# Optimization experiments

Measured on AMD Instinct MI355X. Metric: run time of the kernel, lower is better.

## Reference

```python
import jax, jax.numpy as jnp
import numpy as np

B, S, D, H = 32, 1024, 192, 8
DH = D // H  # 24


def setup_inputs() -> dict:
    key = jax.random.key(0)
    ks = jax.random.split(key, 8)
    s_in = 1.0 / np.sqrt(D)
    return {
        "x": jax.random.normal(ks[0], (B, S, D), dtype=jnp.float32),
        "mask": jax.random.randint(ks[1], (B, S), 0, 2).astype(bool),
        "Wq": jax.random.normal(ks[2], (H, D, DH), dtype=jnp.float32) * s_in,
        "bq": jnp.zeros((H, DH), dtype=jnp.float32),
        "Wk": jax.random.normal(ks[3], (H, D, DH), dtype=jnp.float32) * s_in,
        "bk": jnp.zeros((H, DH), dtype=jnp.float32),
        "Wv": jax.random.normal(ks[4], (H, D, DH), dtype=jnp.float32) * s_in,
        "bv": jnp.zeros((H, DH), dtype=jnp.float32),
        "Wo": jax.random.normal(ks[5], (D, D), dtype=jnp.float32) * s_in,
        "bo": jnp.zeros((D,), dtype=jnp.float32),
    }


def reference(x, mask, Wq, bq, Wk, bk, Wv, bv, Wo, bo):
    # Batched per-head projections: [B,S,D] x [H,D,DH] -> [B,H,S,DH]
    q = jnp.einsum("bsd,hde->bhse", x, Wq) + bq[None, :, None, :]
    k = jnp.einsum("bsd,hde->bhse", x, Wk) + bk[None, :, None, :]
    v = jnp.einsum("bsd,hde->bhse", x, Wv) + bv[None, :, None, :]
    scale = 1.0 / np.sqrt(DH).astype(np.float32)
    scores = jnp.einsum("bhse,bhte->bhst", q, k) * scale  # [B,H,S,S]
    # mask [B,S] broadcast over heads and query positions (masked_fill with -1e9)
    scores = jnp.where(mask[:, None, None, :], scores, -1e9)
    weights = jax.nn.softmax(scores, axis=-1)
    out = jnp.einsum("bhst,bhte->bhse", weights, v)  # [B,H,S,DH]
    # concat heads along last dim -> [B,S,D]
    out = out.transpose(0, 2, 1, 3).reshape(B, S, D)
    return out @ Wo + bo
```

## Files before the change

### kernel.cpp

```cpp
#include <hip/hip_runtime.h>

typedef __attribute__((ext_vector_type(8))) short short8;
typedef __attribute__((ext_vector_type(4))) short short4v;
typedef __attribute__((ext_vector_type(4))) float f32x4;
typedef __attribute__((ext_vector_type(16))) float f32x16;
typedef __attribute__((ext_vector_type(2))) unsigned uint2v;
typedef __attribute__((ext_vector_type(4))) unsigned uint4v;

#define MFMA16(a,b,c) __builtin_amdgcn_mfma_f32_16x16x32_bf16((a),(b),(c),0,0,0)
#define MFMA32(a,b,c) __builtin_amdgcn_mfma_f32_32x32x16_bf16((a),(b),(c),0,0,0)

#define BB 32
#define SS 1024
#define DD 192
#define HH 8
#define DHP 32

#define SCALE_Q 0.294468266742895f

__device__ __forceinline__ short nb(float f) {
    __bf16 h = (__bf16)f;
    return __builtin_bit_cast(short, h);
}
__device__ __forceinline__ float bf2f(short s) {
    union { unsigned u; float f; } v; v.u = ((unsigned)(unsigned short)s) << 16;
    return v.f;
}
__device__ __forceinline__ unsigned pk2(float a, float b) {
    unsigned short lo = __builtin_bit_cast(unsigned short, (__bf16)a);
    unsigned short hi = __builtin_bit_cast(unsigned short, (__bf16)b);
    return (unsigned)lo | ((unsigned)hi << 16);
}

__global__ __launch_bounds__(256) void prep_kernel(
    const float* __restrict__ Wq, const float* __restrict__ Wk, const float* __restrict__ Wv,
    const float* __restrict__ Wo,
    short* __restrict__ WqF, short* __restrict__ WkF, short* __restrict__ WvF,
    short* __restrict__ WoFh, short* __restrict__ WoFl)
{
    int idx = blockIdx.x * 256 + threadIdx.x;
    const int NWX   = 3 * HH * DHP * DD;
    const int NWO   = DD * DD;
    if (idx < NWX) {
        int j = idx;
        int mat = j / (HH * DHP * DD);
        int jj  = j % (HH * DHP * DD);
        int h   = jj / (DHP * DD);
        int rem = jj % (DHP * DD);
        int e   = rem / DD;
        int d   = rem % DD;
        const float* W = (mat == 0) ? Wq : (mat == 1) ? Wk : Wv;
        short* WF      = (mat == 0) ? WqF : (mat == 1) ? WkF : WvF;
        float val = (e < 24) ? W[(h * DD + d) * 24 + e] : 0.f;
        int nt = e & 1, cc = e >> 1;
        int kk = d >> 5, g = (d >> 3) & 3, ee = d & 7;
        WF[(size_t)((((h*2+nt)*6 + kk)*64) + g*16 + cc)*8 + ee] = nb(val);
    } else if (idx < NWX + NWO) {
        int j = idx - NWX;
        int n = j / DD, k = j % DD;
        float f = Wo[k * DD + n];
        short hi = nb(f);
        int nn = n >> 4, cc = n & 15;
        int kk = k >> 5, g = (k >> 3) & 3, ee = k & 7;
        size_t addr = (size_t)(((nn*6 + kk)*64) + g*16 + cc)*8 + ee;
        WoFh[addr] = hi;
        WoFl[addr] = nb(f - bf2f(hi));
    }
}

__global__ __launch_bounds__(1024) void scan_kernel(
    const void* __restrict__ mask_raw,
    float* __restrict__ maskf, int* __restrict__ inv, int* __restrict__ cnt)
{
    int b = blockIdx.x, t = threadIdx.x;
    int lane = t & 63, wv = t >> 6;
    int idx = b * SS + t;

    const unsigned* mw = (const unsigned*)mask_raw;
    bool all01 = true, allf = true;
    #pragma unroll
    for (int i = 0; i < 16; i++) {
        unsigned w = mw[i];
        all01 = all01 && (w <= 1u);
        allf  = allf  && (w == 0u || w == 0x3F800000u);
    }
    bool m;
    if (all01)      m = (mw[idx] != 0u);
    else if (allf)  m = (((const float*)mask_raw)[idx] != 0.f);
    else            m = (((const unsigned char*)mask_raw)[idx] != 0);
    maskf[idx] = m ? 1.f : 0.f;

    unsigned long long bal = __ballot(m);
    int preU  = __popcll(bal & ((1ull << lane) - 1ull));
    int waveU = __popcll(bal);
    __shared__ int wsu[16];
    if (lane == 0) wsu[wv] = waveU;
    __syncthreads();
    int waveOffU = 0, totalU = 0;
    #pragma unroll
    for (int i = 0; i < 16; i++) {
        int v = wsu[i];
        if (i < wv) waveOffU += v;
        totalU += v;
    }
    int posU = waveOffU + preU;
    int posM = totalU + (wv * 64 - waveOffU) + (lane - preU);
    inv[idx] = m ? posU : posM;
    if (t == 0) cnt[b] = totalU;
}

__global__ __launch_bounds__(256) void proj_kernel(
    const float* __restrict__ x,
    const float* __restrict__ bq, const float* __restrict__ bk, const float* __restrict__ bv,
    const short* __restrict__ WqF, const short* __restrict__ WkF, const short* __restrict__ WvF,
    const float* __restrict__ maskf, const int* __restrict__ inv,
    short* __restrict__ Q, short* __restrict__ K, short* __restrict__ Vc)
{
    int tid = threadIdx.x;
    int lane = tid & 63, w = tid >> 6;
    int c = lane & 15, g = lane >> 4;
    int r0 = blockIdx.x * 64 + w * 16;
    int arow = r0 + c;
    int h0 = blockIdx.y * 2;

    int b_ = r0 >> 10;
    int s0 = (r0 & 1023) + g * 4;

    short8 a[6];
    #pragma unroll
    for (int kk = 0; kk < 6; kk++) {
        const float* px = x + (size_t)arow * DD + kk * 32 + g * 8;
        float4 f0 = *(const float4*)px;
        float4 f1 = *(const float4*)(px + 4);
        short8 t;
        t[0]=nb(f0.x); t[1]=nb(f0.y); t[2]=nb(f0.z); t[3]=nb(f0.w);
        t[4]=nb(f1.x); t[5]=nb(f1.y); t[6]=nb(f1.z); t[7]=nb(f1.w);
        a[kk] = t;
    }

    float mrow[4];
    int dst[4];
    #pragma unroll
    for (int r = 0; r < 4; r++) {
        mrow[r] = maskf[b_ * SS + s0 + r];
        dst[r]  = inv[b_ * SS + s0 + r];
    }

    #pragma unroll
    for (int hh = 0; hh < 2; hh++) {
        int h = h0 + hh;
        int bh = b_ * HH + h;
        #pragma unroll
        for (int mat = 0; mat < 3; mat++) {
            const short* WF   = (mat==0)?WqF:(mat==1)?WkF:WvF;
            const float* bias = (mat==0)?bq:(mat==1)?bk:bv;

            f32x4 acc0 = {0.f,0.f,0.f,0.f};
            f32x4 acc1 = {0.f,0.f,0.f,0.f};
            const short* Wp0 = WF + (size_t)((h*2+0)*6) * 512 + lane * 8;
            const short* Wp1 = WF + (size_t)((h*2+1)*6) * 512 + lane * 8;
            #pragma unroll
            for (int kk = 0; kk < 6; kk++) {
                short8 b0 = *(const short8*)(Wp0 + kk * 512);
                short8 b1 = *(const short8*)(Wp1 + kk * 512);
                acc0 = MFMA16(a[kk], b0, acc0);
                acc1 = MFMA16(a[kk], b1, acc1);
            }
            float bv0 = 0.f, bv1 = 0.f;
            if (2*c < 24) {
                float2 bb = *(const float2*)(bias + h * 24 + 2 * c);
                bv0 = bb.x; bv1 = bb.y;
            }

            if (mat == 0) {
                #pragma unroll
                for (int r = 0; r < 4; r++) {
                    float v0 = (acc0[r] + bv0) * SCALE_Q;
                    float v1 = (c == 15) ? 1.0f : (acc1[r] + bv1) * SCALE_Q;
                    *(unsigned*)(Q + ((size_t)bh * SS + s0 + r) * DHP + 2*c) = pk2(v0, v1);
                }
            } else if (mat == 1) {
                #pragma unroll
                for (int r = 0; r < 4; r++) {
                    float v0 = acc0[r] + bv0;
                    float v1 = (c == 15) ? ((mrow[r] != 0.f) ? 0.f : -1e30f)
                                         : (acc1[r] + bv1);
                    *(unsigned*)(K + ((size_t)bh * SS + dst[r]) * DHP + 2*c) = pk2(v0, v1);
                }
            } else {
                #pragma unroll
                for (int r = 0; r < 4; r++) {
                    float v0 = (c == 12) ? 1.0f : (acc0[r] + bv0);
                    float v1 = acc1[r] + bv1;
                    *(unsigned*)(Vc + ((size_t)bh * SS + dst[r]) * DHP + 2*c) = pk2(v0, v1);
                }
            }
        }
    }
}

__global__ __launch_bounds__(256) void vtrans_kernel(
    const short* __restrict__ Vc, short* __restrict__ Vt)
{
    __shared__ short tile[256][33];
    int bh = blockIdx.x, c4 = blockIdx.y;
    int t = threadIdx.x;
    const short* src = Vc + ((size_t)bh * SS + c4 * 256 + t) * DHP;
    short8 a0 = *(const short8*)(src);
    short8 a1 = *(const short8*)(src + 8);
    short8 a2 = *(const short8*)(src + 16);
    short8 a3 = *(const short8*)(src + 24);
    #pragma unroll
    for (int i = 0; i < 8; i++) {
        tile[t][i]      = a0[i];
        tile[t][8 + i]  = a1[i];
        tile[t][16 + i] = a2[i];
        tile[t][24 + i] = a3[i];
    }
    __syncthreads();
    int e = t & 31, jg = t >> 5;
    if (e < 25) {
        short* dstp = Vt + ((size_t)bh * DHP + e) * SS + c4 * 256 + jg * 32;
        short8 o[4];
        #pragma unroll
        for (int i = 0; i < 32; i++) o[i >> 3][i & 7] = tile[jg * 32 + i][e];
        #pragma unroll
        for (int i = 0; i < 4; i++) *(short8*)(dstp + i * 8) = o[i];
    }
}

__device__ __forceinline__ void fproc(const f32x16& S, f32x16& acc,
                                      short8 v0, short8 v1)
{
    float p[16];
    #pragma unroll
    for (int r = 0; r < 16; r++) p[r] = __builtin_amdgcn_exp2f(S[r]);

    unsigned c01 = pk2(p[0],  p[1]);
    unsigned c23 = pk2(p[2],  p[3]);
    unsigned c45 = pk2(p[4],  p[5]);
    unsigned c67 = pk2(p[6],  p[7]);
    unsigned c89 = pk2(p[8],  p[9]);
    unsigned cab = pk2(p[10], p[11]);
    unsigned ccd = pk2(p[12], p[13]);
    unsigned cef = pk2(p[14], p[15]);

    uint2v s0 = __builtin_amdgcn_permlane32_swap(c01, c45, false, false);
    uint2v s1 = __builtin_amdgcn_permlane32_swap(c23, c67, false, false);
    uint2v s2 = __builtin_amdgcn_permlane32_swap(c89, ccd, false, false);
    uint2v s3 = __builtin_amdgcn_permlane32_swap(cab, cef, false, false);

    uint4v w0v = { s0.x, s1.x, s0.y, s1.y };
    uint4v w1v = { s2.x, s3.x, s2.y, s3.y };
    short8 pa0 = __builtin_bit_cast(short8, w0v);
    short8 pa1 = __builtin_bit_cast(short8, w1v);

    acc = MFMA32(pa0, v0, acc);
    acc = MFMA32(pa1, v1, acc);
}

__global__ __launch_bounds__(256) void flash_kernel(
    const short* __restrict__ Q, const short* __restrict__ K, const short* __restrict__ Vt,
    const int* __restrict__ cnt, short* __restrict__ Af)
{
    __shared__ float llds[4][2][32];

    int idx = blockIdx.x;
    int bh = idx & 255;
    int qb = idx >> 8;
    int b = bh >> 3, h = bh & 7;

    int tid = threadIdx.x;
    int lane = tid & 63, w = tid >> 6;
    int l31 = lane & 31;
    int hi = lane >> 5;

    int nt = (cnt[b] + 31) >> 5;

    int qrA = qb * 256 + w * 32;
    int qrB = qrA + 128;

    const short* QpA = Q + ((size_t)bh * SS + qrA + l31) * DHP + hi * 8;
    const short* QpB = Q + ((size_t)bh * SS + qrB + l31) * DHP + hi * 8;
    short8 qA0 = *(const short8*)QpA;
    short8 qA1 = *(const short8*)(QpA + 16);
    short8 qB0 = *(const short8*)QpB;
    short8 qB1 = *(const short8*)(QpB + 16);

    const short* Kp = K + ((size_t)bh * SS + l31) * DHP + hi * 8;
    const short* Vp = Vt + ((size_t)bh * DHP + l31) * SS + hi * 8;

    f32x16 accA, accB, Z16;
    #pragma unroll
    for (int r = 0; r < 16; r++) { accA[r] = 0.f; accB[r] = 0.f; Z16[r] = 0.f; }

    for (int kt = 0; kt < nt; kt++) {
        short8 k0 = *(const short8*)(Kp);
        short8 k1 = *(const short8*)(Kp + 16);
        short8 v0 = *(const short8*)(Vp);
        short8 v1 = *(const short8*)(Vp + 16);
        Kp += 32 * DHP;
        Vp += 32;

        f32x16 SA = MFMA32(k0, qA0, Z16);
        SA = MFMA32(k1, qA1, SA);
        f32x16 SB = MFMA32(k0, qB0, Z16);
        SB = MFMA32(k1, qB1, SB);

        fproc(SA, accA, v0, v1);
        fproc(SB, accB, v0, v1);
    }

    if (l31 == 24) {
        #pragma unroll
        for (int r = 0; r < 16; r++) {
            int row = (r & 3) + 8 * (r >> 2) + 4 * hi;
            llds[w][0][row] = __builtin_amdgcn_rcpf(accA[r]);
            llds[w][1][row] = __builtin_amdgcn_rcpf(accB[r]);
        }
    }
    __builtin_amdgcn_wave_barrier();

    if (l31 < 24) {
        int d = h * 24 + l31;
        int grpA = (b * SS + qrA) >> 4;
        int grpB = (b * SS + qrB) >> 4;
        size_t fcol = (size_t)((d >> 5) * 4 + ((d >> 3) & 3)) * 128 + (d & 7);
        short* opA = Af + (size_t)grpA * 3072 + fcol;
        short* opB = Af + (size_t)grpB * 3072 + fcol;
        #pragma unroll
        for (int r = 0; r < 16; r++) {
            int row = (r & 3) + 8 * (r >> 2) + 4 * hi;
            size_t off = (size_t)(r >> 3) * 3072 + (size_t)(row & 15) * 8;
            opA[off] = nb(accA[r] * llds[w][0][row]);
            opB[off] = nb(accB[r] * llds[w][1][row]);
        }
    }
}

__global__ __launch_bounds__(256) void final_kernel(
    const short* __restrict__ Af,
    const short* __restrict__ WoFh, const short* __restrict__ WoFl,
    const float* __restrict__ bo, float* __restrict__ out)
{
    int tid = threadIdx.x;
    int lane = tid & 63, w = tid >> 6;
    int c = lane & 15, g = lane >> 4;
    int r0 = blockIdx.x * 64 + w * 16;
    int n0 = blockIdx.y * 3;

    short8 a[6];
    #pragma unroll
    for (int kk = 0; kk < 6; kk++)
        a[kk] = *(const short8*)(Af + ((size_t)(r0 >> 4) * 24 + kk*4 + g) * 128 + c * 8);

    f32x4 acc[3];
    #pragma unroll
    for (int n = 0; n < 3; n++) acc[n] = (f32x4){0.f,0.f,0.f,0.f};

    #pragma unroll
    for (int kk = 0; kk < 6; kk++) {
        #pragma unroll
        for (int n = 0; n < 3; n++) {
            const short* bh_p = WoFh + (size_t)((n0+n)*6 + kk) * 512 + lane * 8;
            const short* bl_p = WoFl + (size_t)((n0+n)*6 + kk) * 512 + lane * 8;
            short8 bh = *(const short8*)bh_p;
            short8 bl = *(const short8*)bl_p;
            acc[n] = MFMA16(a[kk], bh, acc[n]);
            acc[n] = MFMA16(a[kk], bl, acc[n]);
        }
    }

    #pragma unroll
    for (int n = 0; n < 3; n++) {
        int col = (n0+n)*16 + c;
        float bv = bo[col];
        #pragma unroll
        for (int r = 0; r < 4; r++) {
            out[(size_t)(r0 + g*4 + r) * DD + col] = acc[n][r] + bv;
        }
    }
}

extern "C" void kernel_launch(void* const* d_in, const int* in_sizes, int n_in,
                              void* d_out, int out_size, void* d_ws, size_t ws_size,
                              hipStream_t stream)
{
    const float* x    = (const float*)d_in[0];
    const void*  mask = d_in[1];
    const float* Wq   = (const float*)d_in[2];
    const float* bq   = (const float*)d_in[3];
    const float* Wk   = (const float*)d_in[4];
    const float* bk   = (const float*)d_in[5];
    const float* Wv   = (const float*)d_in[6];
    const float* bv   = (const float*)d_in[7];
    const float* Wo   = (const float*)d_in[8];
    const float* bo   = (const float*)d_in[9];
    float* out = (float*)d_out;

    char* ws = (char*)d_ws;
    size_t off = 0;
    float* maskf = (float*)(ws + off); off += (size_t)BB*SS*4;
    short* Q     = (short*)(ws + off); off += (size_t)BB*HH*SS*DHP*2;
    short* K     = (short*)(ws + off); off += (size_t)BB*HH*SS*DHP*2;
    short* Vt    = (short*)(ws + off); off += (size_t)BB*HH*SS*DHP*2;
    short* Af    = (short*)(ws + off); off += (size_t)BB*SS*DD*2;
    short* WqF   = (short*)(ws + off); off += (size_t)HH*DHP*DD*2;
    short* WkF   = (short*)(ws + off); off += (size_t)HH*DHP*DD*2;
    short* WvF   = (short*)(ws + off); off += (size_t)HH*DHP*DD*2;
    short* WoFh  = (short*)(ws + off); off += (size_t)DD*DD*2;
    short* WoFl  = (short*)(ws + off); off += (size_t)DD*DD*2;
    short* Vc    = (short*)(ws + off); off += (size_t)BB*HH*SS*DHP*2;
    int*   inv   = (int*)  (ws + off); off += (size_t)BB*SS*4;
    int*   cnt   = (int*)  (ws + off); off += 256;

    prep_kernel<<<dim3(720), dim3(256), 0, stream>>>(
        Wq, Wk, Wv, Wo, WqF, WkF, WvF, WoFh, WoFl);
    scan_kernel<<<dim3(BB), dim3(1024), 0, stream>>>(mask, maskf, inv, cnt);
    proj_kernel<<<dim3(512, 4), dim3(256), 0, stream>>>(
        x, bq, bk, bv, WqF, WkF, WvF, maskf, inv, Q, K, Vc);
    vtrans_kernel<<<dim3(256, 4), dim3(256), 0, stream>>>(Vc, Vt);
    flash_kernel<<<dim3(1024), dim3(256), 0, stream>>>(
        Q, K, Vt, cnt, Af);
    final_kernel<<<dim3(512, 4), dim3(256), 0, stream>>>(
        Af, WoFh, WoFl, bo, out);
}
```

Baseline: 109.4 us.

## Store K and V in MFMA fragment order for contiguous per-lane loads

The K projection output and the V transpose output are now written in a fragment-major layout: each 32-key tile occupies 1024 contiguous shorts, and each lane's short8 operand sits at lane*8. The flash kernel's K and V loads therefore become fully contiguous 16-byte-per-lane loads instead of strided row reads. This aims to cut memory transactions in the attention inner loop. The cost is more scattered writes in the projection and transpose kernels.

```diff
diff --git a/kernel.cpp b/kernel.cpp
--- a/kernel.cpp
+++ b/kernel.cpp
@@ -114,7 +114,7 @@
     const float* __restrict__ bq, const float* __restrict__ bk, const float* __restrict__ bv,
     const short* __restrict__ WqF, const short* __restrict__ WkF, const short* __restrict__ WvF,
     const float* __restrict__ maskf, const int* __restrict__ inv,
-    short* __restrict__ Q, short* __restrict__ K, short* __restrict__ Vc)
+    short* __restrict__ Q, short* __restrict__ KF, short* __restrict__ Vc)
 {
     int tid = threadIdx.x;
     int lane = tid & 63, w = tid >> 6;
@@ -185,7 +185,12 @@
                     float v0 = acc0[r] + bv0;
                     float v1 = (c == 15) ? ((mrow[r] != 0.f) ? 0.f : -1e30f)
                                          : (acc1[r] + bv1);
-                    *(unsigned*)(K + ((size_t)bh * SS + dst[r]) * DHP + 2*c) = pk2(v0, v1);
+                    int d = dst[r];
+                    size_t koff = (size_t)bh * SS * DHP + (size_t)(d >> 5) * 1024
+                                + (size_t)(c >> 3) * 512
+                                + (size_t)((((c >> 2) & 1) * 32) + (d & 31)) * 8
+                                + ((2 * c) & 7);
+                    *(unsigned*)(KF + koff) = pk2(v0, v1);
                 }
             } else {
                 #pragma unroll
@@ -200,7 +205,7 @@
 }
 
 __global__ __launch_bounds__(256) void vtrans_kernel(
-    const short* __restrict__ Vc, short* __restrict__ Vt)
+    const short* __restrict__ Vc, short* __restrict__ VF)
 {
     __shared__ short tile[256][33];
     int bh = blockIdx.x, c4 = blockIdx.y;
@@ -218,14 +223,18 @@
         tile[t][24 + i] = a3[i];
     }
     __syncthreads();
-    int e = t & 31, jg = t >> 5;
-    if (e < 25) {
-        short* dstp = Vt + ((size_t)bh * DHP + e) * SS + c4 * 256 + jg * 32;
-        short8 o[4];
-        #pragma unroll
-        for (int i = 0; i < 32; i++) o[i >> 3][i & 7] = tile[jg * 32 + i][e];
-        #pragma unroll
-        for (int i = 0; i < 4; i++) *(short8*)(dstp + i * 8) = o[i];
+    int L = t & 63, q = t >> 6;
+    int l31 = L & 31, hi = L >> 5;
+    short* outb = VF + (size_t)bh * SS * DHP + (size_t)c4 * 8192;
+    #pragma unroll
+    for (int jj = 0; jj < 4; jj++) {
+        int job = q * 4 + jj;
+        int tt = job >> 1, ii = job & 1;
+        short8 o;
+        #pragma unroll
+        for (int j = 0; j < 8; j++)
+            o[j] = tile[tt * 32 + ii * 16 + hi * 8 + j][l31];
+        *(short8*)(outb + (size_t)tt * 1024 + ii * 512 + (size_t)L * 8) = o;
     }
 }
 
@@ -260,7 +269,7 @@
 }
 
 __global__ __launch_bounds__(256) void flash_kernel(
-    const short* __restrict__ Q, const short* __restrict__ K, const short* __restrict__ Vt,
+    const short* __restrict__ Q, const short* __restrict__ KF, const short* __restrict__ VF,
     const int* __restrict__ cnt, short* __restrict__ Af)
 {
     __shared__ float llds[4][2][32];
@@ -287,8 +296,8 @@
     short8 qB0 = *(const short8*)QpB;
     short8 qB1 = *(const short8*)(QpB + 16);
 
-    const short* Kp = K + ((size_t)bh * SS + l31) * DHP + hi * 8;
-    const short* Vp = Vt + ((size_t)bh * DHP + l31) * SS + hi * 8;
+    const short* Kp = KF + (size_t)bh * SS * DHP + (size_t)lane * 8;
+    const short* Vp = VF + (size_t)bh * SS * DHP + (size_t)lane * 8;
 
     f32x16 accA, accB, Z16;
     #pragma unroll
@@ -296,11 +305,11 @@
 
     for (int kt = 0; kt < nt; kt++) {
         short8 k0 = *(const short8*)(Kp);
-        short8 k1 = *(const short8*)(Kp + 16);
+        short8 k1 = *(const short8*)(Kp + 512);
         short8 v0 = *(const short8*)(Vp);
-        short8 v1 = *(const short8*)(Vp + 16);
-        Kp += 32 * DHP;
-        Vp += 32;
+        short8 v1 = *(const short8*)(Vp + 512);
+        Kp += 1024;
+        Vp += 1024;
 
         f32x16 SA = MFMA32(k0, qA0, Z16);
         SA = MFMA32(k1, qA1, SA);
@@ -402,8 +411,8 @@
     size_t off = 0;
     float* maskf = (float*)(ws + off); off += (size_t)BB*SS*4;
     short* Q     = (short*)(ws + off); off += (size_t)BB*HH*SS*DHP*2;
-    short* K     = (short*)(ws + off); off += (size_t)BB*HH*SS*DHP*2;
-    short* Vt    = (short*)(ws + off); off += (size_t)BB*HH*SS*DHP*2;
+    short* KF    = (short*)(ws + off); off += (size_t)BB*HH*SS*DHP*2;
+    short* VF    = (short*)(ws + off); off += (size_t)BB*HH*SS*DHP*2;
     short* Af    = (short*)(ws + off); off += (size_t)BB*SS*DD*2;
     short* WqF   = (short*)(ws + off); off += (size_t)HH*DHP*DD*2;
     short* WkF   = (short*)(ws + off); off += (size_t)HH*DHP*DD*2;
@@ -418,10 +427,10 @@
         Wq, Wk, Wv, Wo, WqF, WkF, WvF, WoFh, WoFl);
     scan_kernel<<<dim3(BB), dim3(1024), 0, stream>>>(mask, maskf, inv, cnt);
     proj_kernel<<<dim3(512, 4), dim3(256), 0, stream>>>(
-        x, bq, bk, bv, WqF, WkF, WvF, maskf, inv, Q, K, Vc);
-    vtrans_kernel<<<dim3(256, 4), dim3(256), 0, stream>>>(Vc, Vt);
+        x, bq, bk, bv, WqF, WkF, WvF, maskf, inv, Q, KF, Vc);
+    vtrans_kernel<<<dim3(256, 4), dim3(256), 0, stream>>>(Vc, VF);
     flash_kernel<<<dim3(1024), dim3(256), 0, stream>>>(
-        Q, K, Vt, cnt, Af);
+        Q, KF, VF, cnt, Af);
     final_kernel<<<dim3(512, 4), dim3(256), 0, stream>>>(
         Af, WoFh, WoFl, bo, out);
 }
```

Result: no change. 110.8 us (+1.3%).
